# Kernel optimization log

Hardware: AMD Instinct MI355X
Metric: run time of the kernel (lower is better)

## Reference

```python
import jax, jax.numpy as jnp
import numpy as np

N, K, H, E_IN = 4096, 48, 128, 384
SCALE = 30.0
EPS = 1e-5


def _gelu(x):
    return jax.nn.gelu(x, approximate=False)


def _ln(x, s, o):
    m = jnp.mean(x, axis=-1, keepdims=True)
    v = jnp.var(x, axis=-1, keepdims=True)
    return (x - m) * jax.lax.rsqrt(v + EPS) * s + o


def setup_inputs() -> dict:
    key = jax.random.key(0)
    ks = jax.random.split(key, 12)
    init = lambda k, shp: (jax.random.normal(k, shp, jnp.float32) * 0.02)
    return {
        "h_V": jax.random.normal(ks[0], (N, H), jnp.float32),
        "h_E": jax.random.normal(ks[1], (N, K, E_IN), jnp.float32),
        "mask_V": jnp.ones((N,), jnp.float32),
        "mask_attend": jnp.ones((N, K), jnp.float32),
        "W1_w": init(ks[2], (H + E_IN, H)), "W1_b": jnp.zeros((H,), jnp.float32),
        "W2_w": init(ks[3], (H, H)), "W2_b": jnp.zeros((H,), jnp.float32),
        "W3_w": init(ks[4], (H, H)), "W3_b": jnp.zeros((H,), jnp.float32),
        "Win_w": init(ks[5], (H, 4 * H)), "Win_b": jnp.zeros((4 * H,), jnp.float32),
        "Wout_w": init(ks[6], (4 * H, H)), "Wout_b": jnp.zeros((H,), jnp.float32),
        "norm1_s": jnp.ones((H,), jnp.float32), "norm1_o": jnp.zeros((H,), jnp.float32),
        "norm2_s": jnp.ones((H,), jnp.float32), "norm2_o": jnp.zeros((H,), jnp.float32),
    }


def reference(h_V, h_E, mask_V, mask_attend,
              W1_w, W1_b, W2_w, W2_b, W3_w, W3_b,
              Win_w, Win_b, Wout_w, Wout_b,
              norm1_s, norm1_o, norm2_s, norm2_o):
    # expand node features over K neighbors and concat with edge features: [N,K,H+E_IN]
    h_V_expand = jnp.broadcast_to(h_V[:, None, :], (h_V.shape[0], h_E.shape[1], h_V.shape[1]))
    h_EV = jnp.concatenate([h_V_expand, h_E], axis=-1)
    # 3-layer GELU MLP on each edge token
    h = _gelu(jnp.einsum('nke,eh->nkh', h_EV, W1_w) + W1_b)
    h = _gelu(jnp.einsum('nkh,hg->nkg', h, W2_w) + W2_b)
    h_message = jnp.einsum('nkg,gh->nkh', h, W3_w) + W3_b
    # masked sum-reduce over neighbors
    h_message = mask_attend[..., None] * h_message
    dh = jnp.sum(h_message, axis=-2) / SCALE
    h_Vn = _ln(h_V + dh, norm1_s, norm1_o)  # dropout rate = 0.0 -> identity
    # position-wise FFN
    dh = _gelu(h_Vn @ Win_w + Win_b) @ Wout_w + Wout_b
    h_Vn = _ln(h_Vn + dh, norm2_s, norm2_o)
    return mask_V[:, None] * h_Vn
```

## Files before the change

### kernel.cpp

```cpp
#include <hip/hip_runtime.h>
#include <hip/hip_bf16.h>
#include <math.h>

typedef __attribute__((ext_vector_type(8))) __bf16 bf16x8;
typedef __attribute__((ext_vector_type(4))) float f32x4;

#define OFF_W1P    0
#define OFF_W2P    65536
#define OFF_W3P    81920
#define OFF_WINP   98304
#define OFF_WOUTP  163840
#define NPACK      229376
#define OFF_DH_BYTES 458752

__device__ __forceinline__ float gelu_f(float x) {
  float t = 1.5957691216f * x * (1.0f + 0.044715f * x * x);
  return __fdividef(x, 1.0f + __expf(-t));
}

__device__ __forceinline__ bf16x8 cvt8(float4 u, float4 v) {
  bf16x8 r;
  r[0] = (__bf16)u.x; r[1] = (__bf16)u.y; r[2] = (__bf16)u.z; r[3] = (__bf16)u.w;
  r[4] = (__bf16)v.x; r[5] = (__bf16)v.y; r[6] = (__bf16)v.z; r[7] = (__bf16)v.w;
  return r;
}

__device__ __forceinline__ void gload_lds16(const void* g, void* l) {
  __builtin_amdgcn_global_load_lds(
      (const __attribute__((address_space(1))) void*)g,
      (__attribute__((address_space(3))) void*)l, 16, 0, 0);
}

#define MFMA __builtin_amdgcn_mfma_f32_16x16x32_bf16

__global__ __launch_bounds__(256) void prep_kernel(
    const float* __restrict__ W1, const float* __restrict__ W2,
    const float* __restrict__ W3, const float* __restrict__ Wi,
    const float* __restrict__ Wo, __bf16* __restrict__ wsb)
{
  int i = blockIdx.x * 256 + threadIdx.x;
  float v;
  if (i < 65536) {
    int j = i;
    int jj = j & 7, ln = (j >> 3) & 63, n = (j >> 9) & 7, ks = j >> 12;
    int k = ks * 32 + (ln >> 4) * 8 + jj, h = n * 16 + (ln & 15);
    v = W1[k * 128 + h];
  } else if (i < 81920) {
    int j = i - 65536;
    int jj = j & 7, ln = (j >> 3) & 63, n = (j >> 9) & 7, ks = j >> 12;
    int k = ks * 32 + (ln >> 4) * 8 + jj, g = n * 16 + (ln & 15);
    v = W2[k * 128 + g];
  } else if (i < 98304) {
    int j = i - 81920;
    int jj = j & 7, ln = (j >> 3) & 63, n = (j >> 9) & 7, ks = j >> 12;
    int k = ks * 32 + (ln >> 4) * 8 + jj, h = n * 16 + (ln & 15);
    v = W3[k * 128 + h];
  } else if (i < 163840) {
    int j = i - 98304;
    int jj = j & 7, ln = (j >> 3) & 63, n = (j >> 9) & 31, ks = j >> 14;
    int k = ks * 32 + (ln >> 4) * 8 + jj, o = n * 16 + (ln & 15);
    v = Wi[k * 512 + o];
  } else {
    int j = i - 163840;
    int jj = j & 7, ln = (j >> 3) & 63, n = (j >> 9) & 7, ks = j >> 12;
    int k = ks * 32 + (ln >> 4) * 8 + jj, h = n * 16 + (ln & 15);
    v = Wo[k * 128 + h];
  }
  wsb[i] = (__bf16)v;
}

__global__ __launch_bounds__(256, 3) void edge_mlp_kernel(
    const float* __restrict__ hE, const float* __restrict__ hV,
    const float* __restrict__ mask_att, const __bf16* __restrict__ wsb,
    const float* __restrict__ b1, const float* __restrict__ b2,
    const float* __restrict__ b3, float* __restrict__ dh)
{
  __shared__ char lds[36864];

  const int tid = threadIdx.x;
  const int w = tid >> 6, lane = tid & 63;
  const int lo = lane & 15, hi = lane >> 4;
  const int n0 = blockIdx.x * 2;

  const __bf16* W1p = wsb + OFF_W1P;

  f32x4 acc[2][3][2];
#pragma unroll
  for (int nl = 0; nl < 2; nl++)
#pragma unroll
    for (int m = 0; m < 3; m++)
#pragma unroll
      for (int nn = 0; nn < 2; nn++) {
        acc[nl][m][nn][0] = 0.f; acc[nl][m][nn][1] = 0.f;
        acc[nl][m][nn][2] = 0.f; acc[nl][m][nn][3] = 0.f;
      }

  const char* gsrc[3];
  int ldst[3];
#pragma unroll
  for (int j = 0; j < 3; j++) {
    int o = w * 3072 + j * 1024 + lane * 16;
    int r = o >> 7;
    int p = (o >> 4) & 7;
    int lcol = p ^ (r & 7);
    int nl = (r >= 48) ? 1 : 0, kk = r - nl * 48;
    gsrc[j] = (const char*)(hE + (size_t)((n0 + nl) * 48 + kk) * 384 + lcol * 4);
    ldst[j] = w * 3072 + j * 1024;
  }

  bf16x8 bbs[3][2];

#define STAGE(ch, buf) \
  { _Pragma("unroll") for (int j = 0; j < 3; j++) \
      gload_lds16(gsrc[j] + (ch) * 128, &lds[(buf) * 12288 + ldst[j]]); }
#define BBLOAD(ch, set) \
  { _Pragma("unroll") for (int nn = 0; nn < 2; nn++) \
      bbs[set][nn] = *(const bf16x8*)(W1p + ((((ch) + 4) * 8 + w * 2 + nn) << 9) + lane * 8); }

  STAGE(0, 0); BBLOAD(0, 0); STAGE(1, 1); BBLOAD(1, 1); STAGE(2, 2);

#pragma unroll 1
  for (int ks = 0; ks < 4; ++ks) {
    const float* v0 = hV + (n0)     * 128 + ks * 32 + hi * 8;
    const float* v1 = hV + (n0 + 1) * 128 + ks * 32 + hi * 8;
    bf16x8 a0 = cvt8(*(const float4*)v0, *(const float4*)(v0 + 4));
    bf16x8 a1 = cvt8(*(const float4*)v1, *(const float4*)(v1 + 4));
#pragma unroll
    for (int nn = 0; nn < 2; nn++) {
      bf16x8 b = *(const bf16x8*)(W1p + ((ks * 8 + w * 2 + nn) << 9) + lane * 8);
#pragma unroll
      for (int m = 0; m < 3; m++) {
        acc[0][m][nn] = MFMA(a0, b, acc[0][m][nn], 0, 0, 0);
        acc[1][m][nn] = MFMA(a1, b, acc[1][m][nn], 0, 0, 0);
      }
    }
  }

  const int swz0 = (2 * hi) ^ (lo & 7);
  const int swz1 = (2 * hi + 1) ^ (lo & 7);

#pragma unroll
  for (int i = 0; i < 12; ++i) {
    if (i <= 9)       asm volatile("s_waitcnt vmcnt(8)\n\ts_barrier" ::: "memory");
    else if (i == 10) asm volatile("s_waitcnt vmcnt(5)\n\ts_barrier" ::: "memory");
    else              asm volatile("s_waitcnt vmcnt(0)\n\ts_barrier" ::: "memory");

    {
      const char* Ab = lds + (i % 3) * 12288;
      bf16x8 a[2][3];
#pragma unroll
      for (int nl = 0; nl < 2; nl++)
#pragma unroll
        for (int m = 0; m < 3; m++) {
          int r = nl * 48 + m * 16 + lo;
          const char* rb = Ab + r * 128;
          float4 u = *(const float4*)(rb + swz0 * 16);
          float4 v = *(const float4*)(rb + swz1 * 16);
          a[nl][m] = cvt8(u, v);
        }
#pragma unroll
      for (int nn = 0; nn < 2; nn++)
#pragma unroll
        for (int nl = 0; nl < 2; nl++)
#pragma unroll
          for (int m = 0; m < 3; m++)
            acc[nl][m][nn] = MFMA(a[nl][m], bbs[i % 3][nn], acc[nl][m][nn], 0, 0, 0);
    }

    asm volatile("s_waitcnt lgkmcnt(0)\n\ts_barrier" ::: "memory");
    if (i + 2 <= 11) BBLOAD(i + 2, (i + 2) % 3);
    if (i + 3 <= 11) STAGE(i + 3, i % 3);
  }

#pragma unroll 1
  for (int layer = 0; layer < 2; ++layer) {
    const float*  bv = layer ? b2 : b1;
    const __bf16* Wp = wsb + (layer ? OFF_W3P : OFF_W2P);
    __syncthreads();
#pragma unroll
    for (int nn = 0; nn < 2; nn++) {
      int col = (w * 2 + nn) * 16 + lo;
      float bc = bv[col];
#pragma unroll
      for (int nl = 0; nl < 2; nl++)
#pragma unroll
        for (int m = 0; m < 3; m++)
#pragma unroll
          for (int i = 0; i < 4; i++) {
            int row = nl * 48 + m * 16 + hi * 4 + i;
            float g = gelu_f(acc[nl][m][nn][i] + bc);
            *(__bf16*)(lds + row * 256 + ((col * 2) ^ ((row & 7) << 4))) = (__bf16)g;
            acc[nl][m][nn][i] = 0.f;
          }
    }
    __syncthreads();
#pragma unroll 1
    for (int kc2 = 0; kc2 < 2; ++kc2) {
#pragma unroll
      for (int ks32 = 0; ks32 < 2; ++ks32) {
        int ks = kc2 * 2 + ks32;
        bf16x8 bb[2];
#pragma unroll
        for (int nn = 0; nn < 2; nn++)
          bb[nn] = *(const bf16x8*)(Wp + ((ks * 8 + w * 2 + nn) << 9) + lane * 8);
        bf16x8 a[2][3];
#pragma unroll
        for (int nl = 0; nl < 2; nl++)
#pragma unroll
          for (int m = 0; m < 3; m++) {
            int row = nl * 48 + m * 16 + lo;
            a[nl][m] = *(const bf16x8*)(lds + row * 256 + ((kc2 * 128 + ks32 * 64 + hi * 16) ^ ((row & 7) << 4)));
          }
#pragma unroll
        for (int nn = 0; nn < 2; nn++)
#pragma unroll
          for (int nl = 0; nl < 2; nl++)
#pragma unroll
            for (int m = 0; m < 3; m++)
              acc[nl][m][nn] = MFMA(a[nl][m], bb[nn], acc[nl][m][nn], 0, 0, 0);
      }
    }
  }

#pragma unroll
  for (int nl = 0; nl < 2; nl++) {
    float msk[12];
#pragma unroll
    for (int m = 0; m < 3; m++)
#pragma unroll
      for (int i = 0; i < 4; i++)
        msk[m * 4 + i] = mask_att[(n0 + nl) * 48 + m * 16 + hi * 4 + i];
#pragma unroll
    for (int nn = 0; nn < 2; nn++) {
      int col = (w * 2 + nn) * 16 + lo;
      float bc = b3[col];
      float s = 0.f;
#pragma unroll
      for (int m = 0; m < 3; m++)
#pragma unroll
        for (int i = 0; i < 4; i++)
          s += (acc[nl][m][nn][i] + bc) * msk[m * 4 + i];
      s += __shfl_xor(s, 16);
      s += __shfl_xor(s, 32);
      if (hi == 0)
        dh[(n0 + nl) * 128 + col] = s * (1.0f / 30.0f);
    }
  }
#undef STAGE
#undef BBLOAD
}

__global__ __launch_bounds__(256, 2) void node_ffn_kernel(
    const float* __restrict__ hV, const float* __restrict__ maskV,
    const __bf16* __restrict__ wsb, const float* __restrict__ dh,
    const float* __restrict__ Winb, const float* __restrict__ Woutb,
    const float* __restrict__ ns1, const float* __restrict__ no1,
    const float* __restrict__ ns2, const float* __restrict__ no2,
    float* __restrict__ out)
{
  __shared__ char lds2[36864];
  char*  xA  = lds2;
  float* hvn = (float*)(lds2 + 4096);
  char*  A2  = lds2 + 12288;
  float* red = (float*)(lds2 + 28672);

  const __bf16* Winp  = wsb + OFF_WINP;
  const __bf16* Woutp = wsb + OFF_WOUTP;

  const int tid = threadIdx.x;
  const int w = tid >> 6, lane = tid & 63;
  const int lo = lane & 15, hi = lane >> 4;
  const int n0 = blockIdx.x * 16;

  const int row = tid >> 4;
  const int sg  = tid & 15;
  const int node = n0 + row;

  {
    const float* pv = hV + node * 128 + sg * 8;
    const float* pd = dh + node * 128 + sg * 8;
    float4 a0 = *(const float4*)pv;
    float4 a1 = *(const float4*)(pv + 4);
    float4 d0 = *(const float4*)pd;
    float4 d1 = *(const float4*)(pd + 4);
    float x[8] = { a0.x + d0.x, a0.y + d0.y, a0.z + d0.z, a0.w + d0.w,
                   a1.x + d1.x, a1.y + d1.y, a1.z + d1.z, a1.w + d1.w };
    float s = 0.f, sq = 0.f;
#pragma unroll
    for (int j = 0; j < 8; j++) { s += x[j]; sq += x[j] * x[j]; }
#pragma unroll
    for (int off = 8; off >= 1; off >>= 1) { s += __shfl_xor(s, off); sq += __shfl_xor(sq, off); }
    float mean = s * (1.f / 128.f);
    float var  = sq * (1.f / 128.f) - mean * mean;
    float rs = rsqrtf(var + 1e-5f);
    bf16x8 vb;
    float yv[8];
#pragma unroll
    for (int j = 0; j < 8; j++) {
      int col = sg * 8 + j;
      float y = (x[j] - mean) * rs * ns1[col] + no1[col];
      yv[j] = y; vb[j] = (__bf16)y;
    }
    *(float4*)(hvn + row * 128 + sg * 8)     = make_float4(yv[0], yv[1], yv[2], yv[3]);
    *(float4*)(hvn + row * 128 + sg * 8 + 4) = make_float4(yv[4], yv[5], yv[6], yv[7]);
    *(bf16x8*)(xA + row * 256 + ((sg * 16) ^ ((row & 7) << 4))) = vb;
  }
  __syncthreads();

  f32x4 acc[8];
#pragma unroll
  for (int n = 0; n < 8; n++) { acc[n][0] = 0.f; acc[n][1] = 0.f; acc[n][2] = 0.f; acc[n][3] = 0.f; }
#pragma unroll
  for (int ks = 0; ks < 4; ks++) {
    const int kb = (ks * 32 + hi * 8) * 2;
    bf16x8 a = *(const bf16x8*)(xA + lo * 256 + (kb ^ ((lo & 7) << 4)));
#pragma unroll
    for (int n = 0; n < 8; n++) {
      int ng = w * 8 + n;
      bf16x8 b = *(const bf16x8*)(Winp + ((ks * 32 + ng) << 9) + lane * 8);
      acc[n] = MFMA(a, b, acc[n], 0, 0, 0);
    }
  }
#pragma unroll
  for (int n = 0; n < 8; n++) {
    int col = w * 128 + n * 16 + lo;
    float bc = Winb[col];
#pragma unroll
    for (int i = 0; i < 4; i++) {
      int r2 = hi * 4 + i;
      float g = gelu_f(acc[n][i] + bc);
      *(__bf16*)(A2 + r2 * 1024 + ((col * 2) ^ ((r2 & 7) << 4))) = (__bf16)g;
    }
  }
  __syncthreads();

  f32x4 acc2[2];
  acc2[0][0] = 0.f; acc2[0][1] = 0.f; acc2[0][2] = 0.f; acc2[0][3] = 0.f;
  acc2[1][0] = 0.f; acc2[1][1] = 0.f; acc2[1][2] = 0.f; acc2[1][3] = 0.f;
#pragma unroll
  for (int ks = 0; ks < 16; ks++) {
    const int kb = (ks * 32 + hi * 8) * 2;
    bf16x8 a = *(const bf16x8*)(A2 + lo * 1024 + (kb ^ ((lo & 7) << 4)));
#pragma unroll
    for (int n = 0; n < 2; n++) {
      int ng = w * 2 + n;
      bf16x8 b = *(const bf16x8*)(Woutp + ((ks * 8 + ng) << 9) + lane * 8);
      acc2[n] = MFMA(a, b, acc2[n], 0, 0, 0);
    }
  }
#pragma unroll
  for (int n = 0; n < 2; n++) {
    int col = w * 32 + n * 16 + lo;
    float bc = Woutb[col];
#pragma unroll
    for (int i = 0; i < 4; i++) {
      int r2 = hi * 4 + i;
      red[r2 * 128 + col] = acc2[n][i] + bc;
    }
  }
  __syncthreads();

  {
    const float* ph = hvn + row * 128 + sg * 8;
    const float* pr = red + row * 128 + sg * 8;
    float4 h0 = *(const float4*)ph;
    float4 h1 = *(const float4*)(ph + 4);
    float4 r0 = *(const float4*)pr;
    float4 r1 = *(const float4*)(pr + 4);
    float x[8] = { h0.x + r0.x, h0.y + r0.y, h0.z + r0.z, h0.w + r0.w,
                   h1.x + r1.x, h1.y + r1.y, h1.z + r1.z, h1.w + r1.w };
    float s = 0.f, sq = 0.f;
#pragma unroll
    for (int j = 0; j < 8; j++) { s += x[j]; sq += x[j] * x[j]; }
#pragma unroll
    for (int off = 8; off >= 1; off >>= 1) { s += __shfl_xor(s, off); sq += __shfl_xor(sq, off); }
    float mean = s * (1.f / 128.f);
    float var  = sq * (1.f / 128.f) - mean * mean;
    float rs = rsqrtf(var + 1e-5f);
    float mv = maskV[node];
    float o[8];
#pragma unroll
    for (int j = 0; j < 8; j++) {
      int col = sg * 8 + j;
      o[j] = mv * ((x[j] - mean) * rs * ns2[col] + no2[col]);
    }
    *(float4*)(out + node * 128 + sg * 8)     = make_float4(o[0], o[1], o[2], o[3]);
    *(float4*)(out + node * 128 + sg * 8 + 4) = make_float4(o[4], o[5], o[6], o[7]);
  }
}

extern "C" void kernel_launch(void* const* d_in, const int* in_sizes, int n_in,
                              void* d_out, int out_size, void* d_ws, size_t ws_size,
                              hipStream_t stream)
{
  (void)in_sizes; (void)n_in; (void)out_size; (void)ws_size;
  const float* hV   = (const float*)d_in[0];
  const float* hE   = (const float*)d_in[1];
  const float* mV   = (const float*)d_in[2];
  const float* mAtt = (const float*)d_in[3];
  const float* W1   = (const float*)d_in[4];
  const float* b1   = (const float*)d_in[5];
  const float* W2   = (const float*)d_in[6];
  const float* b2   = (const float*)d_in[7];
  const float* W3   = (const float*)d_in[8];
  const float* b3   = (const float*)d_in[9];
  const float* Win  = (const float*)d_in[10];
  const float* binb = (const float*)d_in[11];
  const float* Wout = (const float*)d_in[12];
  const float* bout = (const float*)d_in[13];
  const float* ns1  = (const float*)d_in[14];
  const float* no1  = (const float*)d_in[15];
  const float* ns2  = (const float*)d_in[16];
  const float* no2  = (const float*)d_in[17];

  __bf16* wsb = (__bf16*)d_ws;
  float* dh   = (float*)((char*)d_ws + OFF_DH_BYTES);
  float* out  = (float*)d_out;

  prep_kernel<<<NPACK / 256, 256, 0, stream>>>(W1, W2, W3, Win, Wout, wsb);
  edge_mlp_kernel<<<2048, 256, 0, stream>>>(hE, hV, mAtt, wsb, b1, b2, b3, dh);
  node_ffn_kernel<<<256, 256, 0, stream>>>(hV, mV, wsb, dh, binb, bout,
                                           ns1, no1, ns2, no2, out);
}
```

Before: 115.7 us.

## Stage edge features by 16-row groups with double buffering in first MLP layer

The first edge-MLP layer no longer streams the 96-row edge tile in twelve 32-column chunks through a triple buffer. It now stages whole 16-row by 384-column groups into a double-buffered 48KB LDS region and runs the full K loop per group. The aim is fewer barriers and larger contiguous transfers. The costs are that the W1 fragments are reloaded from global memory in the inner loop for every group, and each group has only two independent MFMA accumulator chains. The larger LDS footprint may also limit occupancy.

```diff
diff --git a/kernel.cpp b/kernel.cpp
--- a/kernel.cpp
+++ b/kernel.cpp
@@ -75,7 +75,7 @@
     const float* __restrict__ b1, const float* __restrict__ b2,
     const float* __restrict__ b3, float* __restrict__ dh)
 {
-  __shared__ char lds[36864];
+  __shared__ char lds[49152];
 
   const int tid = threadIdx.x;
   const int w = tid >> 6, lane = tid & 63;
@@ -95,29 +95,23 @@
         acc[nl][m][nn][2] = 0.f; acc[nl][m][nn][3] = 0.f;
       }
 
-  const char* gsrc[3];
-  int ldst[3];
-#pragma unroll
-  for (int j = 0; j < 3; j++) {
-    int o = w * 3072 + j * 1024 + lane * 16;
-    int r = o >> 7;
-    int p = (o >> 4) & 7;
-    int lcol = p ^ (r & 7);
-    int nl = (r >= 48) ? 1 : 0, kk = r - nl * 48;
-    gsrc[j] = (const char*)(hE + (size_t)((n0 + nl) * 48 + kk) * 384 + lcol * 4);
-    ldst[j] = w * 3072 + j * 1024;
-  }
-
-  bf16x8 bbs[3][2];
-
-#define STAGE(ch, buf) \
-  { _Pragma("unroll") for (int j = 0; j < 3; j++) \
-      gload_lds16(gsrc[j] + (ch) * 128, &lds[(buf) * 12288 + ldst[j]]); }
-#define BBLOAD(ch, set) \
-  { _Pragma("unroll") for (int nn = 0; nn < 2; nn++) \
-      bbs[set][nn] = *(const bf16x8*)(W1p + ((((ch) + 4) * 8 + w * 2 + nn) << 9) + lane * 8); }
-
-  STAGE(0, 0); BBLOAD(0, 0); STAGE(1, 1); BBLOAD(1, 1); STAGE(2, 2);
+  int srcoff[6];
+#pragma unroll
+  for (int q = 0; q < 6; q++) {
+    int p = q * 4096 + tid * 16;
+    int r = p / 1536;
+    int u = (p - r * 1536) >> 4;
+    int ul = (u & ~7) | ((u & 7) ^ (r & 7));
+    srcoff[q] = r * 384 + ul * 4;
+  }
+  const float* gb[6];
+#pragma unroll
+  for (int g = 0; g < 6; g++)
+    gb[g] = hE + ((size_t)(n0 + g / 3) * 48 + (g % 3) * 16) * 384;
+
+#define STAGE(g) \
+  { _Pragma("unroll") for (int q = 0; q < 6; q++) \
+      gload_lds16(gb[g] + srcoff[q], &lds[((g) & 1) * 24576 + q * 4096 + w * 1024]); }
 
 #pragma unroll 1
   for (int ks = 0; ks < 4; ++ks) {
@@ -136,41 +130,33 @@
     }
   }
 
-  const int swz0 = (2 * hi) ^ (lo & 7);
-  const int swz1 = (2 * hi + 1) ^ (lo & 7);
-
-#pragma unroll
-  for (int i = 0; i < 12; ++i) {
-    if (i <= 9)       asm volatile("s_waitcnt vmcnt(8)\n\ts_barrier" ::: "memory");
-    else if (i == 10) asm volatile("s_waitcnt vmcnt(5)\n\ts_barrier" ::: "memory");
-    else              asm volatile("s_waitcnt vmcnt(0)\n\ts_barrier" ::: "memory");
-
-    {
-      const char* Ab = lds + (i % 3) * 12288;
-      bf16x8 a[2][3];
-#pragma unroll
-      for (int nl = 0; nl < 2; nl++)
-#pragma unroll
-        for (int m = 0; m < 3; m++) {
-          int r = nl * 48 + m * 16 + lo;
-          const char* rb = Ab + r * 128;
-          float4 u = *(const float4*)(rb + swz0 * 16);
-          float4 v = *(const float4*)(rb + swz1 * 16);
-          a[nl][m] = cvt8(u, v);
-        }
-#pragma unroll
-      for (int nn = 0; nn < 2; nn++)
-#pragma unroll
-        for (int nl = 0; nl < 2; nl++)
-#pragma unroll
-          for (int m = 0; m < 3; m++)
-            acc[nl][m][nn] = MFMA(a[nl][m], bbs[i % 3][nn], acc[nl][m][nn], 0, 0, 0);
-    }
-
+  STAGE(0);
+
+#pragma unroll 1
+  for (int g = 0; g < 6; ++g) {
     asm volatile("s_waitcnt lgkmcnt(0)\n\ts_barrier" ::: "memory");
-    if (i + 2 <= 11) BBLOAD(i + 2, (i + 2) % 3);
-    if (i + 3 <= 11) STAGE(i + 3, i % 3);
-  }
+    if (g < 5) STAGE(g + 1);
+    if (g < 5) asm volatile("s_waitcnt vmcnt(6)\n\ts_barrier" ::: "memory");
+    else       asm volatile("s_waitcnt vmcnt(0)\n\ts_barrier" ::: "memory");
+
+    const char* Ab = lds + (g & 1) * 24576;
+    const int nl = g / 3, m = g % 3;
+    const char* rb = Ab + lo * 1536;
+#pragma unroll
+    for (int ks = 0; ks < 12; ++ks) {
+      int u0 = ks * 8 + ((hi * 2) ^ (lo & 7));
+      int u1 = ks * 8 + ((hi * 2 + 1) ^ (lo & 7));
+      float4 fu = *(const float4*)(rb + u0 * 16);
+      float4 fv = *(const float4*)(rb + u1 * 16);
+      bf16x8 a = cvt8(fu, fv);
+#pragma unroll
+      for (int nn = 0; nn < 2; nn++) {
+        bf16x8 b = *(const bf16x8*)(W1p + (((4 + ks) * 8 + w * 2 + nn) << 9) + lane * 8);
+        acc[nl][m][nn] = MFMA(a, b, acc[nl][m][nn], 0, 0, 0);
+      }
+    }
+  }
+#undef STAGE
 
 #pragma unroll 1
   for (int layer = 0; layer < 2; ++layer) {
@@ -246,8 +232,6 @@
         dh[(n0 + nl) * 128 + col] = s * (1.0f / 30.0f);
     }
   }
-#undef STAGE
-#undef BBLOAD
 }
 
 __global__ __launch_bounds__(256, 2) void node_ffn_kernel(
```

New measurement: 320.0 us. 2.77x slower.
